# Performance work log

Hardware: AMD Instinct MI355X
Metric: run time of the kernel (lower is better)

The kernel has to match this reference:

```python
import jax, jax.numpy as jnp
import numpy as np

B, L, E, D, H, N_ENT = 64, 50, 50, 100, 100, 200000


def setup_inputs() -> dict:
    key = jax.random.key(0)
    ks = jax.random.split(key, 12)
    neighbor_ids = jax.random.randint(ks[0], (B, L, E), 0, N_ENT)
    # 0/1 adjacency; mimic GraphConstructer: symmetric with self-loops
    adj = jax.random.randint(ks[1], (B, L, E, E), 0, 2).astype(jnp.int32)
    adj = jnp.maximum(adj, adj.transpose(0, 1, 3, 2))
    adj = jnp.maximum(adj, jnp.eye(E, dtype=jnp.int32))
    s = 0.1  # ~ 1/sqrt(D) init scale
    emb = jax.random.normal(ks[2], (N_ENT, D), jnp.float32) * s
    Wq = jax.random.normal(ks[3], (D, H), jnp.float32) * s
    bq = jax.random.normal(ks[4], (H,), jnp.float32) * s
    Wk = jax.random.normal(ks[5], (D, H), jnp.float32) * s
    bk = jax.random.normal(ks[6], (H,), jnp.float32) * s
    Wv = jax.random.normal(ks[7], (D, H), jnp.float32) * s
    bv = jax.random.normal(ks[8], (H,), jnp.float32) * s
    Ws = jax.random.normal(ks[9], (D, H), jnp.float32) * s
    bs = jax.random.normal(ks[10], (H,), jnp.float32) * s
    return {"neighbor_ids": neighbor_ids, "adj": adj, "emb": emb,
            "Wq": Wq, "bq": bq, "Wk": Wk, "bk": bk,
            "Wv": Wv, "bv": bv, "Ws": Ws, "bs": bs}


def reference(neighbor_ids, adj, emb, Wq, bq, Wk, bk, Wv, bv, Ws, bs):
    b, l, e = neighbor_ids.shape
    d = emb.shape[1]
    h = Wq.shape[1]
    # embedding gather: [B,L,E,D] -> [G,E,D], G = B*L graphs
    x = emb[neighbor_ids].reshape(b * l, e, d)
    a = adj.reshape(b * l, e, e)
    # TransformerConv (heads=1): q,k,v linear with bias
    q = x @ Wq + bq
    k = x @ Wk + bk
    v = x @ Wv + bv
    scores = jnp.einsum('gid,gjd->gij', q, k) / jnp.sqrt(jnp.asarray(h, x.dtype))
    # edge (j -> i) exists when adj[j, i] != 0; target i attends over sources j
    mask = a.transpose(0, 2, 1) != 0  # mask[g, i, j]
    neg = jnp.finfo(scores.dtype).min
    attn = jax.nn.softmax(jnp.where(mask, scores, neg), axis=-1)
    # nodes with no incoming edge aggregate to zero (PyG softmax/scatter semantics)
    attn = jnp.where(mask.any(-1, keepdims=True), attn, jnp.zeros((), attn.dtype))
    agg = jnp.einsum('gij,gjd->gid', attn, v)
    out = agg + x @ Ws + bs  # root/skip connection with bias
    # take center node (index 0) of each ego-graph -> [B, L, H]
    return out.reshape(b, l, e, h)[:, :, 0, :]
```

## Files before the change

### kernel.cpp

```cpp
#include <hip/hip_runtime.h>
#include <hip/hip_bf16.h>
#include <math.h>

#define E_N 50
#define D_N 100
#define H_N 100
#define XS_LD 102

__device__ __forceinline__ float bf2f(unsigned int s16) {
    return __uint_as_float(s16 << 16);
}

__device__ __forceinline__ unsigned short f2bf(float f) {
    unsigned int u = __float_as_uint(f);
    unsigned int r = (u + 0x7FFFu + ((u >> 16) & 1u)) >> 16;
    return (unsigned short)r;
}

template <bool F32>
__device__ __forceinline__ float ldx(const void* p, int i) {
    if (F32) return reinterpret_cast<const float*>(p)[i];
    return bf2f(reinterpret_cast<const unsigned short*>(p)[i]);
}

template <bool F32>
__device__ __forceinline__ float4 ld4(const void* p, long long i4) {
    if (F32) return reinterpret_cast<const float4*>(p)[i4];
    uint2 v = reinterpret_cast<const uint2*>(p)[i4];
    float4 f;
    f.x = bf2f(v.x & 0xFFFFu);
    f.y = bf2f(v.x >> 16);
    f.z = bf2f(v.y & 0xFFFFu);
    f.w = bf2f(v.y >> 16);
    return f;
}

__device__ __forceinline__ int detect_f32(const void* emb, int tid, int* flag_s) {
    if (tid < 64) {
        unsigned short hw = reinterpret_cast<const unsigned short*>(emb)[tid * 2];
        float v = bf2f(hw);
        float a = fabsf(v);
        int sane = (v == 0.f) || (a >= 1e-4f && a <= 8.0f);
        unsigned long long ball = __ballot(sane);
        if (tid == 0) *flag_s = (__popcll(ball) < 32) ? 1 : 0;
    }
    __syncthreads();
    return *flag_s;
}

template <bool F32>
__device__ __forceinline__ void prep_core(const void* Wq, const void* bq,
                                          const void* Wk, const void* bv,
                                          const void* bs,
                                          float* Mt, float* c, float* b2,
                                          int blk, int t) {
    if (blk < D_N) {
        if (t < D_N) {
            float acc = 0.f;
            #pragma unroll 10
            for (int h = 0; h < H_N; ++h)
                acc = fmaf(ldx<F32>(Wk, t * H_N + h), ldx<F32>(Wq, blk * H_N + h), acc);
            Mt[blk * D_N + t] = acc;
        }
    } else {
        if (t < D_N) {
            float acc = 0.f;
            #pragma unroll 10
            for (int h = 0; h < H_N; ++h)
                acc = fmaf(ldx<F32>(Wk, t * H_N + h), ldx<F32>(bq, h), acc);
            c[t] = acc;
            b2[t] = ldx<F32>(bs, t) + ldx<F32>(bv, t);
        }
    }
}

__global__ __launch_bounds__(128)
void prep_kernel(const void* __restrict__ emb,
                 const void* __restrict__ Wq, const void* __restrict__ bq,
                 const void* __restrict__ Wk, const void* __restrict__ bv,
                 const void* __restrict__ bs,
                 float* __restrict__ Mt, float* __restrict__ c,
                 float* __restrict__ b2) {
    __shared__ int flag_s;
    int t = threadIdx.x;
    int f32 = detect_f32(emb, t, &flag_s);
    if (f32) prep_core<true>(Wq, bq, Wk, bv, bs, Mt, c, b2, blockIdx.x, t);
    else     prep_core<false>(Wq, bq, Wk, bv, bs, Mt, c, b2, blockIdx.x, t);
}

template <bool F32>
__device__ __forceinline__ void graph_core(
    int g, int sub, int t,
    const int* __restrict__ nbr, const int* __restrict__ adj,
    const void* __restrict__ emb,
    const void* __restrict__ Wv, const void* __restrict__ Ws,
    const void* __restrict__ bv,
    const float* __restrict__ Mt, const float* __restrict__ c,
    const float* __restrict__ b2, void* __restrict__ out,
    unsigned short (*xs)[E_N * XS_LD], float (*x0s)[D_N],
    int (*ids)[E_N], int (*msk)[E_N], float (*us)[D_N],
    float (*ssc)[E_N], float (*attns)[E_N], float (*ys)[D_N], float* den_s)
{
    if (t < E_N) {
        ids[sub][t] = nbr[g * E_N + t];
        msk[sub][t] = adj[(size_t)g * (E_N * E_N) + t * E_N];
    } else if (t >= 64 && t < 64 + 25) {
        int id0 = nbr[g * E_N];
        int q = t - 64;
        float4 f = ld4<F32>(emb, (long long)id0 * (D_N / 4) + q);
        x0s[sub][4 * q + 0] = f.x;
        x0s[sub][4 * q + 1] = f.y;
        x0s[sub][4 * q + 2] = f.z;
        x0s[sub][4 * q + 3] = f.w;
    }
    __syncthreads();

    {
        unsigned int* xw = reinterpret_cast<unsigned int*>(xs[sub]);
        for (int i = t; i < E_N * (D_N / 4); i += 128) {
            int j = i / 25;
            int q = i - j * 25;
            float4 f = ld4<F32>(emb, (long long)ids[sub][j] * (D_N / 4) + q);
            unsigned int w0 = (unsigned int)f2bf(f.x) | ((unsigned int)f2bf(f.y) << 16);
            unsigned int w1 = (unsigned int)f2bf(f.z) | ((unsigned int)f2bf(f.w) << 16);
            int wbase = j * (XS_LD / 2) + 2 * q;
            xw[wbase] = w0;
            xw[wbase + 1] = w1;
        }
    }
    __syncthreads();

    if (t < D_N) {
        float acc = c[t];
        #pragma unroll 10
        for (int e = 0; e < D_N; ++e)
            acc = fmaf(Mt[e * D_N + t], x0s[sub][e], acc);
        us[sub][t] = acc;
    }
    __syncthreads();

    if (t < E_N) {
        const unsigned int* xw = reinterpret_cast<const unsigned int*>(xs[sub])
                                 + t * (XS_LD / 2);
        float acc = 0.f;
        #pragma unroll 10
        for (int d2 = 0; d2 < D_N / 2; ++d2) {
            unsigned int w = xw[d2];
            acc = fmaf(bf2f(w & 0xFFFFu), us[sub][2 * d2], acc);
            acc = fmaf(bf2f(w >> 16),     us[sub][2 * d2 + 1], acc);
        }
        ssc[sub][t] = acc * 0.1f;
    }
    __syncthreads();

    if (t < E_N) {
        float m = -3.0e38f;
        #pragma unroll 10
        for (int j = 0; j < E_N; ++j)
            if (msk[sub][j]) m = fmaxf(m, ssc[sub][j]);
        attns[sub][t] = msk[sub][t] ? __expf(ssc[sub][t] - m) : 0.f;
    }
    __syncthreads();

    if (t < D_N) {
        float den = 0.f;
        #pragma unroll 10
        for (int j = 0; j < E_N; ++j) den += attns[sub][j];
        float inv = den > 0.f ? 1.0f / den : 0.f;
        float acc = 0.f;
        #pragma unroll 10
        for (int j = 0; j < E_N; ++j) {
            float xv = bf2f(xs[sub][j * XS_LD + t]);
            acc = fmaf(attns[sub][j], xv, acc);
        }
        ys[sub][t] = acc * inv;
        if (t == 0) den_s[sub] = den;
    }
    __syncthreads();

    if (t < H_N) {
        float acc = b2[t];
        if (!(den_s[sub] > 0.f)) acc -= ldx<F32>(bv, t);
        #pragma unroll 10
        for (int d = 0; d < D_N; ++d) {
            acc = fmaf(ys[sub][d],  ldx<F32>(Wv, d * H_N + t), acc);
            acc = fmaf(x0s[sub][d], ldx<F32>(Ws, d * H_N + t), acc);
        }
        size_t o = (size_t)g * H_N + t;
        if (F32) reinterpret_cast<float*>(out)[o] = acc;
        else     reinterpret_cast<unsigned short*>(out)[o] = f2bf(acc);
    }
}

__global__ __launch_bounds__(256)
void graph_enc_kernel(const int* __restrict__ nbr,
                      const int* __restrict__ adj,
                      const void* __restrict__ emb,
                      const void* __restrict__ Wv, const void* __restrict__ Ws,
                      const void* __restrict__ bv,
                      const float* __restrict__ Mt, const float* __restrict__ c,
                      const float* __restrict__ b2,
                      void* __restrict__ out, int G)
{
    __shared__ unsigned short xs[2][E_N * XS_LD];
    __shared__ float x0s[2][D_N];
    __shared__ int   ids[2][E_N];
    __shared__ int   msk[2][E_N];
    __shared__ float us[2][D_N];
    __shared__ float ssc[2][E_N];
    __shared__ float attns[2][E_N];
    __shared__ float ys[2][D_N];
    __shared__ float den_s[2];
    __shared__ int   flag_s;

    const int tid = threadIdx.x;
    const int sub = tid >> 7;
    const int t   = tid & 127;
    const int g   = blockIdx.x * 2 + sub;

    int f32 = detect_f32(emb, tid, &flag_s);
    if (g >= G) {
        for (int i = 0; i < 6; ++i) __syncthreads();
        return;
    }
    if (f32)
        graph_core<true>(g, sub, t, nbr, adj, emb, Wv, Ws, bv, Mt, c, b2, out,
                         xs, x0s, ids, msk, us, ssc, attns, ys, den_s);
    else
        graph_core<false>(g, sub, t, nbr, adj, emb, Wv, Ws, bv, Mt, c, b2, out,
                          xs, x0s, ids, msk, us, ssc, attns, ys, den_s);
}

extern "C" void kernel_launch(void* const* d_in, const int* in_sizes, int n_in,
                              void* d_out, int out_size, void* d_ws, size_t ws_size,
                              hipStream_t stream) {
    const int* nbr = (const int*)d_in[0];
    const int* adj = (const int*)d_in[1];
    const void* emb = d_in[2];
    const void* Wq  = d_in[3];
    const void* bq  = d_in[4];
    const void* Wk  = d_in[5];
    const void* Wv  = d_in[7];
    const void* bv  = d_in[8];
    const void* Ws  = d_in[9];
    const void* bs  = d_in[10];

    float* Mt = (float*)d_ws;
    float* c  = Mt + D_N * D_N;
    float* b2 = c + D_N;

    const int G = in_sizes[0] / E_N;

    prep_kernel<<<D_N + 1, 128, 0, stream>>>(emb, Wq, bq, Wk, bv, bs, Mt, c, b2);
    graph_enc_kernel<<<(G + 1) / 2, 256, 0, stream>>>(
        nbr, adj, emb, Wv, Ws, bv, Mt, c, b2, d_out, G);
}
```

Measured before the change: 191.7 us.

## Process one graph per 64-thread wavefront block with register-batched gathers

New measurement: 195.9 us. 1.02x slower.

```diff
diff --git a/kernel.cpp b/kernel.cpp
--- a/kernel.cpp
+++ b/kernel.cpp
@@ -90,109 +90,142 @@
 
 template <bool F32>
 __device__ __forceinline__ void graph_core(
-    int g, int sub, int t,
+    int g, int lane,
     const int* __restrict__ nbr, const int* __restrict__ adj,
     const void* __restrict__ emb,
     const void* __restrict__ Wv, const void* __restrict__ Ws,
     const void* __restrict__ bv,
     const float* __restrict__ Mt, const float* __restrict__ c,
     const float* __restrict__ b2, void* __restrict__ out,
-    unsigned short (*xs)[E_N * XS_LD], float (*x0s)[D_N],
-    int (*ids)[E_N], int (*msk)[E_N], float (*us)[D_N],
-    float (*ssc)[E_N], float (*attns)[E_N], float (*ys)[D_N], float* den_s)
+    unsigned short* xs, float* x0s, int* ids, int* msk,
+    float* us, float* ssc, float* attns, float* ys, float* den_s)
 {
-    if (t < E_N) {
-        ids[sub][t] = nbr[g * E_N + t];
-        msk[sub][t] = adj[(size_t)g * (E_N * E_N) + t * E_N];
-    } else if (t >= 64 && t < 64 + 25) {
-        int id0 = nbr[g * E_N];
-        int q = t - 64;
-        float4 f = ld4<F32>(emb, (long long)id0 * (D_N / 4) + q);
-        x0s[sub][4 * q + 0] = f.x;
-        x0s[sub][4 * q + 1] = f.y;
-        x0s[sub][4 * q + 2] = f.z;
-        x0s[sub][4 * q + 3] = f.w;
-    }
-    __syncthreads();
-
-    {
-        unsigned int* xw = reinterpret_cast<unsigned int*>(xs[sub]);
-        for (int i = t; i < E_N * (D_N / 4); i += 128) {
-            int j = i / 25;
-            int q = i - j * 25;
-            float4 f = ld4<F32>(emb, (long long)ids[sub][j] * (D_N / 4) + q);
-            unsigned int w0 = (unsigned int)f2bf(f.x) | ((unsigned int)f2bf(f.y) << 16);
-            unsigned int w1 = (unsigned int)f2bf(f.z) | ((unsigned int)f2bf(f.w) << 16);
-            int wbase = j * (XS_LD / 2) + 2 * q;
-            xw[wbase] = w0;
-            xw[wbase + 1] = w1;
-        }
-    }
-    __syncthreads();
-
-    if (t < D_N) {
-        float acc = c[t];
-        #pragma unroll 10
-        for (int e = 0; e < D_N; ++e)
-            acc = fmaf(Mt[e * D_N + t], x0s[sub][e], acc);
-        us[sub][t] = acc;
-    }
-    __syncthreads();
-
-    if (t < E_N) {
-        const unsigned int* xw = reinterpret_cast<const unsigned int*>(xs[sub])
-                                 + t * (XS_LD / 2);
+    if (lane < E_N) ids[lane] = nbr[g * E_N + lane];
+    __syncthreads();
+
+    unsigned int* xw = reinterpret_cast<unsigned int*>(xs);
+
+    float4 bufA[10];
+    #pragma unroll
+    for (int k = 0; k < 10; ++k) {
+        int i = lane + 64 * k;
+        int j = i / 25, q = i - j * 25;
+        bufA[k] = ld4<F32>(emb, (long long)ids[j] * 25 + q);
+    }
+    int mk = (lane < E_N) ? adj[(size_t)g * (E_N * E_N) + lane * E_N] : 0;
+
+    float4 bufB[10];
+    #pragma unroll
+    for (int k = 0; k < 10; ++k) {
+        int i = lane + 64 * (k + 10);
+        if (i < E_N * 25) {
+            int j = i / 25, q = i - j * 25;
+            bufB[k] = ld4<F32>(emb, (long long)ids[j] * 25 + q);
+        }
+    }
+
+    #pragma unroll
+    for (int k = 0; k < 10; ++k) {
+        int i = lane + 64 * k;
+        int j = i / 25, q = i - j * 25;
+        float4 f = bufA[k];
+        xw[j * (XS_LD / 2) + 2 * q]     = (unsigned int)f2bf(f.x) | ((unsigned int)f2bf(f.y) << 16);
+        xw[j * (XS_LD / 2) + 2 * q + 1] = (unsigned int)f2bf(f.z) | ((unsigned int)f2bf(f.w) << 16);
+    }
+    if (lane < 25) {
+        float4 f = bufA[0];
+        x0s[4 * lane + 0] = f.x; x0s[4 * lane + 1] = f.y;
+        x0s[4 * lane + 2] = f.z; x0s[4 * lane + 3] = f.w;
+    }
+    #pragma unroll
+    for (int k = 0; k < 10; ++k) {
+        int i = lane + 64 * (k + 10);
+        if (i < E_N * 25) {
+            int j = i / 25, q = i - j * 25;
+            float4 f = bufB[k];
+            xw[j * (XS_LD / 2) + 2 * q]     = (unsigned int)f2bf(f.x) | ((unsigned int)f2bf(f.y) << 16);
+            xw[j * (XS_LD / 2) + 2 * q + 1] = (unsigned int)f2bf(f.z) | ((unsigned int)f2bf(f.w) << 16);
+        }
+    }
+    if (lane < E_N) msk[lane] = mk;
+    __syncthreads();
+
+    #pragma unroll
+    for (int rep = 0; rep < 2; ++rep) {
+        int d = lane + 64 * rep;
+        if (d < D_N) {
+            float acc = c[d];
+            #pragma unroll 10
+            for (int e = 0; e < D_N; ++e)
+                acc = fmaf(Mt[e * D_N + d], x0s[e], acc);
+            us[d] = acc;
+        }
+    }
+    __syncthreads();
+
+    if (lane < E_N) {
+        const unsigned int* xr = xw + lane * (XS_LD / 2);
         float acc = 0.f;
         #pragma unroll 10
         for (int d2 = 0; d2 < D_N / 2; ++d2) {
-            unsigned int w = xw[d2];
-            acc = fmaf(bf2f(w & 0xFFFFu), us[sub][2 * d2], acc);
-            acc = fmaf(bf2f(w >> 16),     us[sub][2 * d2 + 1], acc);
-        }
-        ssc[sub][t] = acc * 0.1f;
-    }
-    __syncthreads();
-
-    if (t < E_N) {
+            unsigned int w = xr[d2];
+            acc = fmaf(bf2f(w & 0xFFFFu), us[2 * d2], acc);
+            acc = fmaf(bf2f(w >> 16),     us[2 * d2 + 1], acc);
+        }
+        ssc[lane] = acc * 0.1f;
+    }
+    __syncthreads();
+
+    if (lane < E_N) {
         float m = -3.0e38f;
         #pragma unroll 10
         for (int j = 0; j < E_N; ++j)
-            if (msk[sub][j]) m = fmaxf(m, ssc[sub][j]);
-        attns[sub][t] = msk[sub][t] ? __expf(ssc[sub][t] - m) : 0.f;
-    }
-    __syncthreads();
-
-    if (t < D_N) {
+            if (msk[j]) m = fmaxf(m, ssc[j]);
+        attns[lane] = msk[lane] ? __expf(ssc[lane] - m) : 0.f;
+    }
+    __syncthreads();
+
+    {
         float den = 0.f;
         #pragma unroll 10
-        for (int j = 0; j < E_N; ++j) den += attns[sub][j];
+        for (int j = 0; j < E_N; ++j) den += attns[j];
         float inv = den > 0.f ? 1.0f / den : 0.f;
-        float acc = 0.f;
-        #pragma unroll 10
-        for (int j = 0; j < E_N; ++j) {
-            float xv = bf2f(xs[sub][j * XS_LD + t]);
-            acc = fmaf(attns[sub][j], xv, acc);
-        }
-        ys[sub][t] = acc * inv;
-        if (t == 0) den_s[sub] = den;
-    }
-    __syncthreads();
-
-    if (t < H_N) {
-        float acc = b2[t];
-        if (!(den_s[sub] > 0.f)) acc -= ldx<F32>(bv, t);
-        #pragma unroll 10
-        for (int d = 0; d < D_N; ++d) {
-            acc = fmaf(ys[sub][d],  ldx<F32>(Wv, d * H_N + t), acc);
-            acc = fmaf(x0s[sub][d], ldx<F32>(Ws, d * H_N + t), acc);
-        }
-        size_t o = (size_t)g * H_N + t;
-        if (F32) reinterpret_cast<float*>(out)[o] = acc;
-        else     reinterpret_cast<unsigned short*>(out)[o] = f2bf(acc);
-    }
-}
-
-__global__ __launch_bounds__(256)
+        #pragma unroll
+        for (int rep = 0; rep < 2; ++rep) {
+            int d = lane + 64 * rep;
+            if (d < D_N) {
+                float acc = 0.f;
+                #pragma unroll 10
+                for (int j = 0; j < E_N; ++j)
+                    acc = fmaf(attns[j], bf2f(xs[j * XS_LD + d]), acc);
+                ys[d] = acc * inv;
+            }
+        }
+        if (lane == 0) *den_s = den;
+    }
+    __syncthreads();
+
+    {
+        float sneg = (*den_s > 0.f) ? 0.f : 1.f;
+        #pragma unroll
+        for (int rep = 0; rep < 2; ++rep) {
+            int h = lane + 64 * rep;
+            if (h < H_N) {
+                float acc = b2[h] - sneg * ldx<F32>(bv, h);
+                #pragma unroll 10
+                for (int d = 0; d < D_N; ++d) {
+                    acc = fmaf(ys[d],  ldx<F32>(Wv, d * H_N + h), acc);
+                    acc = fmaf(x0s[d], ldx<F32>(Ws, d * H_N + h), acc);
+                }
+                size_t o = (size_t)g * H_N + h;
+                if (F32) reinterpret_cast<float*>(out)[o] = acc;
+                else     reinterpret_cast<unsigned short*>(out)[o] = f2bf(acc);
+            }
+        }
+    }
+}
+
+__global__ __launch_bounds__(64)
 void graph_enc_kernel(const int* __restrict__ nbr,
                       const int* __restrict__ adj,
                       const void* __restrict__ emb,
@@ -200,35 +233,29 @@
                       const void* __restrict__ bv,
                       const float* __restrict__ Mt, const float* __restrict__ c,
                       const float* __restrict__ b2,
-                      void* __restrict__ out, int G)
+                      void* __restrict__ out)
 {
-    __shared__ unsigned short xs[2][E_N * XS_LD];
-    __shared__ float x0s[2][D_N];
-    __shared__ int   ids[2][E_N];
-    __shared__ int   msk[2][E_N];
-    __shared__ float us[2][D_N];
-    __shared__ float ssc[2][E_N];
-    __shared__ float attns[2][E_N];
-    __shared__ float ys[2][D_N];
-    __shared__ float den_s[2];
+    __shared__ unsigned short xs[E_N * XS_LD];
+    __shared__ float x0s[D_N];
+    __shared__ int   ids[E_N];
+    __shared__ int   msk[E_N];
+    __shared__ float us[D_N];
+    __shared__ float ssc[E_N];
+    __shared__ float attns[E_N];
+    __shared__ float ys[D_N];
+    __shared__ float den_s;
     __shared__ int   flag_s;
 
-    const int tid = threadIdx.x;
-    const int sub = tid >> 7;
-    const int t   = tid & 127;
-    const int g   = blockIdx.x * 2 + sub;
-
-    int f32 = detect_f32(emb, tid, &flag_s);
-    if (g >= G) {
-        for (int i = 0; i < 6; ++i) __syncthreads();
-        return;
-    }
+    const int lane = threadIdx.x;
+    const int g    = blockIdx.x;
+
+    int f32 = detect_f32(emb, lane, &flag_s);
     if (f32)
-        graph_core<true>(g, sub, t, nbr, adj, emb, Wv, Ws, bv, Mt, c, b2, out,
-                         xs, x0s, ids, msk, us, ssc, attns, ys, den_s);
+        graph_core<true>(g, lane, nbr, adj, emb, Wv, Ws, bv, Mt, c, b2, out,
+                         xs, x0s, ids, msk, us, ssc, attns, ys, &den_s);
     else
-        graph_core<false>(g, sub, t, nbr, adj, emb, Wv, Ws, bv, Mt, c, b2, out,
-                          xs, x0s, ids, msk, us, ssc, attns, ys, den_s);
+        graph_core<false>(g, lane, nbr, adj, emb, Wv, Ws, bv, Mt, c, b2, out,
+                          xs, x0s, ids, msk, us, ssc, attns, ys, &den_s);
 }
 
 extern "C" void kernel_launch(void* const* d_in, const int* in_sizes, int n_in,
@@ -252,6 +279,6 @@
     const int G = in_sizes[0] / E_N;
 
     prep_kernel<<<D_N + 1, 128, 0, stream>>>(emb, Wq, bq, Wk, bv, bs, Mt, c, b2);
-    graph_enc_kernel<<<(G + 1) / 2, 256, 0, stream>>>(
-        nbr, adj, emb, Wv, Ws, bv, Mt, c, b2, d_out, G);
-}
+    graph_enc_kernel<<<G, 64, 0, stream>>>(nbr, adj, emb, Wv, Ws, bv,
+                                           Mt, c, b2, d_out);
+}
```
